# Optimization experiments

Hardware: AMD Instinct MI355X
Metric: run time of the kernel (lower is better)

Reference implementation:

```python
import jax, jax.numpy as jnp
import numpy as np

D_MODEL = 1024
N_HEADS = 16
HEAD_DIM = D_MODEL // N_HEADS  # 64


def setup_inputs() -> dict:
    key = jax.random.key(0)
    ks = jax.random.split(key, 6)
    scale_in = 1.0 / np.sqrt(D_MODEL)
    scale_hd = 1.0 / np.sqrt(N_HEADS * HEAD_DIM)
    inputs_q = jax.random.normal(ks[0], (4, 2048, D_MODEL), dtype=jnp.float32)
    # DenseGeneral kernels: [d_model, n_heads, head_dim] for q/k/v, [n_heads, head_dim, d_model] for out.
    Wq = jax.random.normal(ks[1], (D_MODEL, N_HEADS, HEAD_DIM), dtype=jnp.float32) * scale_in
    Wk = jax.random.normal(ks[2], (D_MODEL, N_HEADS, HEAD_DIM), dtype=jnp.float32) * scale_in
    Wv = jax.random.normal(ks[3], (D_MODEL, N_HEADS, HEAD_DIM), dtype=jnp.float32) * scale_in
    Wo = jax.random.normal(ks[4], (N_HEADS, HEAD_DIM, D_MODEL), dtype=jnp.float32) * scale_hd
    bq = jnp.zeros((N_HEADS, HEAD_DIM), dtype=jnp.float32)
    bk = jnp.zeros((N_HEADS, HEAD_DIM), dtype=jnp.float32)
    bv = jnp.zeros((N_HEADS, HEAD_DIM), dtype=jnp.float32)
    bo = jnp.zeros((D_MODEL,), dtype=jnp.float32)
    return {"inputs_q": inputs_q, "Wq": Wq, "bq": bq, "Wk": Wk, "bk": bk,
            "Wv": Wv, "bv": bv, "Wo": Wo, "bo": bo}


def reference(inputs_q, Wq, bq, Wk, bk, Wv, bv, Wo, bo):
    # Self-attention: inputs_kv = inputs_q.
    # QKV projections (DenseGeneral axis=-1 -> (heads, head_dim)).
    q = jnp.einsum('bsf,fhd->bshd', inputs_q, Wq) + bq  # [B,S,H,D]
    k = jnp.einsum('bsf,fhd->bshd', inputs_q, Wk) + bk
    v = jnp.einsum('bsf,fhd->bshd', inputs_q, Wv) + bv
    # Scaled dot-product attention (naive: full [B,H,S,S] scores, as in source).
    q = q / jnp.sqrt(jnp.asarray(HEAD_DIM, dtype=q.dtype))
    scores = jnp.einsum('bqhd,bkhd->bhqk', q, k)  # [B,H,Sq,Sk]
    attn = jax.nn.softmax(scores, axis=-1)
    x = jnp.einsum('bhqk,bkhd->bqhd', attn, v)  # [B,S,H,D]
    # Output projection over (heads, head_dim).
    out = jnp.einsum('bqhd,hdf->bqf', x, Wo) + bo  # [B,S,d_model]
    return out
```

## Files before the change

### kernel.cpp

```cpp
#include <hip/hip_runtime.h>
#include <math.h>

typedef __bf16 bf16;
typedef __attribute__((ext_vector_type(4))) __bf16 bf16x4;
typedef __attribute__((ext_vector_type(8))) __bf16 bf16x8;
typedef __attribute__((ext_vector_type(4))) float f32x4;

#define LOG2E 1.44269504088896340736f

__device__ __forceinline__ f32x4 mfma16(bf16x8 a, bf16x8 b, f32x4 c) {
  return __builtin_amdgcn_mfma_f32_16x16x32_bf16(a, b, c, 0, 0, 0);
}

__device__ __forceinline__ void load_lds16(const bf16* g, bf16* l) {
  __builtin_amdgcn_global_load_lds(
      (__attribute__((address_space(1))) void*)(g),
      (__attribute__((address_space(3))) void*)(l), 16, 0, 0);
}

__global__ __launch_bounds__(256) void prep(
    const float* __restrict__ x, const float* __restrict__ Wq,
    const float* __restrict__ Wk, const float* __restrict__ Wv,
    const float* __restrict__ Wo, bf16* __restrict__ xb,
    bf16* __restrict__ Wcat, bf16* __restrict__ WoT, float qscale) {
  __shared__ float t[32][33];
  const int z = blockIdx.z;
  const int tid = threadIdx.x;
  if (z == 4) {
    const int blk = blockIdx.y * 32 + blockIdx.x;
    const int base = blk * 8192;
#pragma unroll
    for (int u = 0; u < 4; u++) {
      int i = base + u * 2048 + tid * 8;
      float4 a = *(const float4*)&x[i];
      float4 b = *(const float4*)&x[i + 4];
      bf16x8 v;
      v[0] = (bf16)a.x; v[1] = (bf16)a.y; v[2] = (bf16)a.z; v[3] = (bf16)a.w;
      v[4] = (bf16)b.x; v[5] = (bf16)b.y; v[6] = (bf16)b.z; v[7] = (bf16)b.w;
      *(bf16x8*)&xb[i] = v;
    }
  } else {
    const float* src = (z == 0) ? Wq : (z == 1) ? Wk : (z == 2) ? Wv : Wo;
    bf16* dst = (z == 3) ? WoT : (Wcat + (size_t)z * 1024 * 1024);
    const float scale = (z == 0) ? qscale : 1.0f;
    const int tx = tid & 31, ty = tid >> 5;
    int c0 = blockIdx.x * 32, r0 = blockIdx.y * 32;
    for (int i = ty; i < 32; i += 8)
      t[i][tx] = src[(r0 + i) * 1024 + c0 + tx];
    __syncthreads();
    for (int i = ty; i < 32; i += 8)
      dst[(c0 + i) * 1024 + r0 + tx] = (bf16)(t[tx][i] * scale);
  }
}

template <int MODE>
__global__ __launch_bounds__(256, 2) void gemm_bt(
    const bf16* __restrict__ A, const bf16* __restrict__ Bt, int N, int K,
    bf16* __restrict__ Qo, bf16* __restrict__ Ko, bf16* __restrict__ Vo,
    const float* __restrict__ b0, const float* __restrict__ b1,
    const float* __restrict__ b2,
    float* __restrict__ Co, const float* __restrict__ bias) {
  __shared__ bf16 lA[128 * 32];
  __shared__ bf16 lB[128 * 32];
  const int tid = threadIdx.x;
  const int lane = tid & 63, w = tid >> 6;
  const int l16 = lane & 15, quad = lane >> 4;
  const int swz = (l16 >> 2) & 3;
  const int wm = w >> 1, wn = w & 1;
  const int id = blockIdx.x;
  const int xcd = id & 7, local = id >> 3;
  const int m0 = (xcd * 8 + (local & 7)) * 128;
  const int n0 = (local >> 3) * 128;

  const int srow = w * 16 + (lane >> 2);
  const int scol = (((lane & 3) ^ ((lane >> 4) & 3)) * 8);
  const bf16* Ag = A + (size_t)(m0 + srow) * K + scol;
  const bf16* Bg = Bt + (size_t)(n0 + srow) * K + scol;
  bf16* lAw = &lA[w * 16 * 32];
  bf16* lBw = &lB[w * 16 * 32];

  f32x4 acc[4][4] = {};
  for (int k0 = 0; k0 < K; k0 += 32) {
    __syncthreads();
    load_lds16(Ag + k0, lAw);
    load_lds16(Ag + k0 + (size_t)64 * K, lAw + 64 * 32);
    load_lds16(Bg + k0, lBw);
    load_lds16(Bg + k0 + (size_t)64 * K, lBw + 64 * 32);
    __syncthreads();
    bf16x8 af[4], bfr[4];
#pragma unroll
    for (int i = 0; i < 4; i++)
      af[i] = *(const bf16x8*)&lA[(wm * 64 + i * 16 + l16) * 32 + (quad ^ swz) * 8];
#pragma unroll
    for (int i = 0; i < 4; i++)
      bfr[i] = *(const bf16x8*)&lB[(wn * 64 + i * 16 + l16) * 32 + (quad ^ swz) * 8];
#pragma unroll
    for (int i = 0; i < 4; i++)
#pragma unroll
      for (int j = 0; j < 4; j++)
        acc[i][j] = mfma16(af[i], bfr[j], acc[i][j]);
  }

  if (MODE == 0) {
    const int which = n0 >> 10;
    bf16* dst = (which == 0) ? Qo : (which == 1) ? Ko : Vo;
    const float* bsrc = (which == 0) ? b0 : (which == 1) ? b1 : b2;
    const float bscale = (which == 0) ? (0.125f * LOG2E) : 1.0f;
    const int ss = (which == 2) ? 1 : 64;
    const int sd = (which == 2) ? 2048 : 1;
#pragma unroll
    for (int j = 0; j < 4; j++) {
      const int nn = (n0 & 1023) + wn * 64 + j * 16 + l16;
      const int h = nn >> 6, d = nn & 63;
      const float bias_v = bsrc[nn] * bscale;
#pragma unroll
      for (int i = 0; i < 4; i++) {
#pragma unroll
        for (int rg = 0; rg < 4; rg++) {
          const int grow = m0 + wm * 64 + i * 16 + quad * 4 + rg;
          const int bb = grow >> 11, s = grow & 2047;
          dst[(size_t)(bb * 16 + h) * 131072 + (size_t)s * ss + d * sd] =
              (bf16)(acc[i][j][rg] + bias_v);
        }
      }
    }
  } else {
#pragma unroll
    for (int j = 0; j < 4; j++) {
      const int gcol = n0 + wn * 64 + j * 16 + l16;
      const float bias_v = bias[gcol];
#pragma unroll
      for (int i = 0; i < 4; i++) {
#pragma unroll
        for (int rg = 0; rg < 4; rg++) {
          const int grow = m0 + wm * 64 + i * 16 + quad * 4 + rg;
          Co[(size_t)grow * N + gcol] = acc[i][j][rg] + bias_v;
        }
      }
    }
  }
}

__global__ __launch_bounds__(256, 2) void attn(const bf16* __restrict__ Q,
                                               const bf16* __restrict__ Kb,
                                               const bf16* __restrict__ Vt,
                                               bf16* __restrict__ X2) {
  __shared__ bf16 lK[2][2][64][32];
  __shared__ bf16 lV[2][2][64][32];
  __shared__ bf16 lP[4][64][72];
  const int tid = threadIdx.x;
  const int lane = tid & 63, w = tid >> 6;
  const int l16 = lane & 15, quad = lane >> 4;
  const int swz = (l16 >> 2) & 3;
  const int bh = blockIdx.x & 63;
  const int q0 = (blockIdx.x >> 6) * 256;
  const int bb = bh >> 4, h = bh & 15;
  const size_t base = (size_t)bh * 2048 * 64;

  bf16x8 aq[4][2];
#pragma unroll
  for (int mi = 0; mi < 4; mi++)
#pragma unroll
    for (int kh = 0; kh < 2; kh++)
      aq[mi][kh] = *(const bf16x8*)&Q[base + (size_t)(q0 + w * 64 + mi * 16 + l16) * 64 + kh * 32 + quad * 8];

  f32x4 o_acc[4][4] = {};
  float l_r[4] = {0.f, 0.f, 0.f, 0.f};

  const int drow = lane >> 2;
  const int dcol = (((lane & 3) ^ ((lane >> 4) & 3)) * 8);
  const bf16* Kg = Kb + base + (size_t)(w * 16 + drow) * 64 + dcol;
  const bf16* Vg = Vt + base + (size_t)(w * 16 + drow) * 2048 + dcol;

  load_lds16(Kg, &lK[0][0][w * 16][0]);
  load_lds16(Kg + 32, &lK[0][1][w * 16][0]);
  load_lds16(Vg, &lV[0][0][w * 16][0]);
  load_lds16(Vg + 32, &lV[0][1][w * 16][0]);

  for (int kt = 0; kt < 32; kt++) {
    const int p = kt & 1;
    __syncthreads();
    if (kt + 1 < 32) {
      const bf16* kg = Kg + (size_t)(kt + 1) * 64 * 64;
      const bf16* vg = Vg + (kt + 1) * 64;
      load_lds16(kg, &lK[p ^ 1][0][w * 16][0]);
      load_lds16(kg + 32, &lK[p ^ 1][1][w * 16][0]);
      load_lds16(vg, &lV[p ^ 1][0][w * 16][0]);
      load_lds16(vg + 32, &lV[p ^ 1][1][w * 16][0]);
    }

#pragma unroll
    for (int g = 0; g < 2; g++) {
      f32x4 s[2][4] = {};
#pragma unroll
      for (int n2 = 0; n2 < 2; n2++) {
        const int ni = g * 2 + n2;
        bf16x8 ak0 = *(const bf16x8*)&lK[p][0][ni * 16 + l16][(quad ^ swz) * 8];
        bf16x8 ak1 = *(const bf16x8*)&lK[p][1][ni * 16 + l16][(quad ^ swz) * 8];
#pragma unroll
        for (int mi = 0; mi < 4; mi++) {
          s[n2][mi] = mfma16(ak0, aq[mi][0], s[n2][mi]);
          s[n2][mi] = mfma16(ak1, aq[mi][1], s[n2][mi]);
        }
      }
#pragma unroll
      for (int n2 = 0; n2 < 2; n2++) {
        const int ni = g * 2 + n2;
#pragma unroll
        for (int mi = 0; mi < 4; mi++) {
          bf16x4 pw;
          float lp = 0.f;
#pragma unroll
          for (int rg = 0; rg < 4; rg++) {
            float pv = __builtin_amdgcn_exp2f(s[n2][mi][rg]);
            lp += pv;
            pw[rg] = (bf16)pv;
          }
          l_r[mi] += lp;
          *(bf16x4*)&lP[w][mi * 16 + l16][ni * 16 + quad * 4] = pw;
        }
      }
    }

    bf16x8 vf0[4], vf1[4];
#pragma unroll
    for (int di = 0; di < 4; di++) {
      vf0[di] = *(const bf16x8*)&lV[p][0][di * 16 + l16][(quad ^ swz) * 8];
      vf1[di] = *(const bf16x8*)&lV[p][1][di * 16 + l16][(quad ^ swz) * 8];
    }
#pragma unroll
    for (int mi = 0; mi < 4; mi++) {
      bf16x8 ap0 = *(const bf16x8*)&lP[w][mi * 16 + l16][quad * 8];
      bf16x8 ap1 = *(const bf16x8*)&lP[w][mi * 16 + l16][32 + quad * 8];
#pragma unroll
      for (int di = 0; di < 4; di++) {
        o_acc[mi][di] = mfma16(ap0, vf0[di], o_acc[mi][di]);
        o_acc[mi][di] = mfma16(ap1, vf1[di], o_acc[mi][di]);
      }
    }
  }

#pragma unroll
  for (int mi = 0; mi < 4; mi++) {
    float l = l_r[mi];
    l += __shfl_xor(l, 16);
    l += __shfl_xor(l, 32);
    l_r[mi] = 1.f / l;
  }
#pragma unroll
  for (int mi = 0; mi < 4; mi++)
#pragma unroll
    for (int rg = 0; rg < 4; rg++) {
      float inv = __shfl(l_r[mi], quad * 4 + rg);
      int s = q0 + w * 64 + mi * 16 + quad * 4 + rg;
#pragma unroll
      for (int di = 0; di < 4; di++) {
        float v = o_acc[mi][di][rg] * inv;
        X2[((size_t)bb * 2048 + s) * 1024 + h * 64 + di * 16 + l16] = (bf16)v;
      }
    }
}

extern "C" void kernel_launch(void* const* d_in, const int* in_sizes, int n_in,
                              void* d_out, int out_size, void* d_ws, size_t ws_size,
                              hipStream_t stream) {
  const float* x  = (const float*)d_in[0];
  const float* Wq = (const float*)d_in[1];
  const float* bq = (const float*)d_in[2];
  const float* Wk = (const float*)d_in[3];
  const float* bk = (const float*)d_in[4];
  const float* Wv = (const float*)d_in[5];
  const float* bv = (const float*)d_in[6];
  const float* Wo = (const float*)d_in[7];
  const float* bo = (const float*)d_in[8];
  float* out = (float*)d_out;

  char* ws = (char*)d_ws;
  bf16* Xb   = (bf16*)(ws);
  bf16* Wcat = (bf16*)(ws + 16777216);
  bf16* WoT  = (bf16*)(ws + 23068672);
  bf16* Qb   = (bf16*)(ws + 25165824);
  bf16* Kbf  = (bf16*)(ws + 41943040);
  bf16* Vt   = (bf16*)(ws + 58720256);
  bf16* X2   = Xb;

  prep<<<dim3(32, 32, 5), 256, 0, stream>>>(
      x, Wq, Wk, Wv, Wo, Xb, Wcat, WoT, 0.125f * LOG2E);

  gemm_bt<0><<<1536, 256, 0, stream>>>(Xb, Wcat, 3072, 1024,
      Qb, Kbf, Vt, bq, bk, bv, nullptr, nullptr);

  attn<<<512, 256, 0, stream>>>(Qb, Kbf, Vt, X2);

  gemm_bt<1><<<512, 256, 0, stream>>>(X2, WoT, 1024, 1024,
      nullptr, nullptr, nullptr, nullptr, nullptr, nullptr, out, bo);
}
```

Baseline: 289.4 us.

## Widen GEMM K-step to 64 and vectorize epilogue stores via swapped MFMA operands

```diff
diff --git a/kernel.cpp b/kernel.cpp
--- a/kernel.cpp
+++ b/kernel.cpp
@@ -54,14 +54,14 @@
 }
 
 template <int MODE>
-__global__ __launch_bounds__(256, 2) void gemm_bt(
+__global__ __launch_bounds__(256, 3) void gemm_bt(
     const bf16* __restrict__ A, const bf16* __restrict__ Bt, int N, int K,
     bf16* __restrict__ Qo, bf16* __restrict__ Ko, bf16* __restrict__ Vo,
     const float* __restrict__ b0, const float* __restrict__ b1,
     const float* __restrict__ b2,
     float* __restrict__ Co, const float* __restrict__ bias) {
-  __shared__ bf16 lA[128 * 32];
-  __shared__ bf16 lB[128 * 32];
+  __shared__ bf16 lA[2][128 * 32];
+  __shared__ bf16 lB[2][128 * 32];
   const int tid = threadIdx.x;
   const int lane = tid & 63, w = tid >> 6;
   const int l16 = lane & 15, quad = lane >> 4;
@@ -76,29 +76,35 @@
   const int scol = (((lane & 3) ^ ((lane >> 4) & 3)) * 8);
   const bf16* Ag = A + (size_t)(m0 + srow) * K + scol;
   const bf16* Bg = Bt + (size_t)(n0 + srow) * K + scol;
-  bf16* lAw = &lA[w * 16 * 32];
-  bf16* lBw = &lB[w * 16 * 32];
+  const int ldw = w * 16 * 32;
 
   f32x4 acc[4][4] = {};
-  for (int k0 = 0; k0 < K; k0 += 32) {
+  for (int k0 = 0; k0 < K; k0 += 64) {
     __syncthreads();
-    load_lds16(Ag + k0, lAw);
-    load_lds16(Ag + k0 + (size_t)64 * K, lAw + 64 * 32);
-    load_lds16(Bg + k0, lBw);
-    load_lds16(Bg + k0 + (size_t)64 * K, lBw + 64 * 32);
+    load_lds16(Ag + k0, &lA[0][ldw]);
+    load_lds16(Ag + k0 + (size_t)64 * K, &lA[0][ldw + 64 * 32]);
+    load_lds16(Ag + k0 + 32, &lA[1][ldw]);
+    load_lds16(Ag + k0 + 32 + (size_t)64 * K, &lA[1][ldw + 64 * 32]);
+    load_lds16(Bg + k0, &lB[0][ldw]);
+    load_lds16(Bg + k0 + (size_t)64 * K, &lB[0][ldw + 64 * 32]);
+    load_lds16(Bg + k0 + 32, &lB[1][ldw]);
+    load_lds16(Bg + k0 + 32 + (size_t)64 * K, &lB[1][ldw + 64 * 32]);
     __syncthreads();
-    bf16x8 af[4], bfr[4];
-#pragma unroll
-    for (int i = 0; i < 4; i++)
-      af[i] = *(const bf16x8*)&lA[(wm * 64 + i * 16 + l16) * 32 + (quad ^ swz) * 8];
-#pragma unroll
-    for (int i = 0; i < 4; i++)
-      bfr[i] = *(const bf16x8*)&lB[(wn * 64 + i * 16 + l16) * 32 + (quad ^ swz) * 8];
-#pragma unroll
-    for (int i = 0; i < 4; i++)
-#pragma unroll
-      for (int j = 0; j < 4; j++)
-        acc[i][j] = mfma16(af[i], bfr[j], acc[i][j]);
+#pragma unroll
+    for (int ks = 0; ks < 2; ks++) {
+      bf16x8 af[4], bfr[4];
+#pragma unroll
+      for (int i = 0; i < 4; i++)
+        af[i] = *(const bf16x8*)&lA[ks][(wm * 64 + i * 16 + l16) * 32 + (quad ^ swz) * 8];
+#pragma unroll
+      for (int i = 0; i < 4; i++)
+        bfr[i] = *(const bf16x8*)&lB[ks][(wn * 64 + i * 16 + l16) * 32 + (quad ^ swz) * 8];
+#pragma unroll
+      for (int i = 0; i < 4; i++)
+#pragma unroll
+        for (int j = 0; j < 4; j++)
+          acc[i][j] = mfma16(bfr[j], af[i], acc[i][j]);
+    }
   }
 
   if (MODE == 0) {
@@ -106,36 +112,42 @@
     bf16* dst = (which == 0) ? Qo : (which == 1) ? Ko : Vo;
     const float* bsrc = (which == 0) ? b0 : (which == 1) ? b1 : b2;
     const float bscale = (which == 0) ? (0.125f * LOG2E) : 1.0f;
-    const int ss = (which == 2) ? 1 : 64;
-    const int sd = (which == 2) ? 2048 : 1;
 #pragma unroll
     for (int j = 0; j < 4; j++) {
-      const int nn = (n0 & 1023) + wn * 64 + j * 16 + l16;
-      const int h = nn >> 6, d = nn & 63;
-      const float bias_v = bsrc[nn] * bscale;
+      const int nn0 = (n0 & 1023) + wn * 64 + j * 16 + quad * 4;
+      const int h = nn0 >> 6, d0 = nn0 & 63;
+      float4 bv4 = *(const float4*)&bsrc[nn0];
 #pragma unroll
       for (int i = 0; i < 4; i++) {
-#pragma unroll
-        for (int rg = 0; rg < 4; rg++) {
-          const int grow = m0 + wm * 64 + i * 16 + quad * 4 + rg;
-          const int bb = grow >> 11, s = grow & 2047;
-          dst[(size_t)(bb * 16 + h) * 131072 + (size_t)s * ss + d * sd] =
-              (bf16)(acc[i][j][rg] + bias_v);
+        const int grow = m0 + wm * 64 + i * 16 + l16;
+        const int bb = grow >> 11, sq = grow & 2047;
+        const size_t hb = (size_t)(bb * 16 + h) * 131072;
+        if (which != 2) {
+          bf16x4 pw;
+          pw[0] = (bf16)(acc[i][j][0] + bv4.x * bscale);
+          pw[1] = (bf16)(acc[i][j][1] + bv4.y * bscale);
+          pw[2] = (bf16)(acc[i][j][2] + bv4.z * bscale);
+          pw[3] = (bf16)(acc[i][j][3] + bv4.w * bscale);
+          *(bf16x4*)&dst[hb + (size_t)sq * 64 + d0] = pw;
+        } else {
+          dst[hb + (size_t)(d0 + 0) * 2048 + sq] = (bf16)(acc[i][j][0] + bv4.x);
+          dst[hb + (size_t)(d0 + 1) * 2048 + sq] = (bf16)(acc[i][j][1] + bv4.y);
+          dst[hb + (size_t)(d0 + 2) * 2048 + sq] = (bf16)(acc[i][j][2] + bv4.z);
+          dst[hb + (size_t)(d0 + 3) * 2048 + sq] = (bf16)(acc[i][j][3] + bv4.w);
         }
       }
     }
   } else {
 #pragma unroll
     for (int j = 0; j < 4; j++) {
-      const int gcol = n0 + wn * 64 + j * 16 + l16;
-      const float bias_v = bias[gcol];
+      const int gcol = n0 + wn * 64 + j * 16 + quad * 4;
+      float4 bv4 = *(const float4*)&bias[gcol];
 #pragma unroll
       for (int i = 0; i < 4; i++) {
-#pragma unroll
-        for (int rg = 0; rg < 4; rg++) {
-          const int grow = m0 + wm * 64 + i * 16 + quad * 4 + rg;
-          Co[(size_t)grow * N + gcol] = acc[i][j][rg] + bias_v;
-        }
+        const int grow = m0 + wm * 64 + i * 16 + l16;
+        f32x4 v = acc[i][j];
+        v[0] += bv4.x; v[1] += bv4.y; v[2] += bv4.z; v[3] += bv4.w;
+        *(f32x4*)&Co[(size_t)grow * N + gcol] = v;
       }
     }
   }
```

New measurement: 282.5 us. 1.02x faster.
